# Optimization experiments

Measured on AMD Instinct MI355X. Metric: run time of the kernel, lower is better.

The kernel has to match this reference:

```python
import jax, jax.numpy as jnp
import numpy as np

NUM_TAGS = 48
B, S = 512, 2048


def setup_inputs() -> dict:
    key = jax.random.key(0)
    k1, k2, k3, k4, k5 = jax.random.split(key, 5)
    emissions = jax.random.normal(k1, (B, S, NUM_TAGS), dtype=jnp.float32)
    tags = jax.random.randint(k2, (B, S), 0, NUM_TAGS, dtype=jnp.int32)
    mask = jnp.ones((B, S), dtype=jnp.float32)
    transitions = jax.random.uniform(k3, (NUM_TAGS, NUM_TAGS), minval=-0.1, maxval=0.1, dtype=jnp.float32)
    start_transitions = jax.random.uniform(k4, (NUM_TAGS,), minval=-0.1, maxval=0.1, dtype=jnp.float32)
    end_transitions = jax.random.uniform(k5, (NUM_TAGS,), minval=-0.1, maxval=0.1, dtype=jnp.float32)
    return {"emissions": emissions, "transitions": transitions,
            "start_transitions": start_transitions, "end_transitions": end_transitions,
            "tags": tags, "mask": mask}


def reference(emissions, transitions, start_transitions, end_transitions, tags, mask):
    # emissions: [B,S,T], tags: [B,S] int, mask: [B,S] float (1 = valid)
    b, s, t = emissions.shape
    barange = jnp.arange(b)

    # ---- gold path score (fully vectorized over time) ----
    emit = jnp.take_along_axis(emissions, tags[:, :, None], axis=2)[..., 0]  # [B,S]
    score = start_transitions[tags[:, 0]] + emit[:, 0]
    trans = transitions[tags[:, :-1], tags[:, 1:]]                            # [B,S-1]
    score = score + jnp.sum((trans + emit[:, 1:]) * mask[:, 1:], axis=1)
    last_idx = mask.sum(axis=1).astype(jnp.int32) - 1
    last_tags = tags[barange, last_idx]
    score = score + end_transitions[last_tags]

    # ---- log-partition via forward algorithm (scan over time) ----
    alpha0 = start_transitions[None, :] + emissions[:, 0]                     # [B,T]

    def step(alpha, xs):
        emit_t, mask_t = xs                                                   # [B,T], [B]
        # scores[b,i,j] = alpha[b,i] + transitions[i,j] + emit_t[b,j]
        scores = alpha[:, :, None] + transitions[None, :, :] + emit_t[:, None, :]
        next_alpha = jax.nn.logsumexp(scores, axis=1)                         # [B,T]
        m = mask_t[:, None]
        alpha = next_alpha * m + alpha * (1.0 - m)
        return alpha, None

    xs = (jnp.swapaxes(emissions[:, 1:], 0, 1), jnp.swapaxes(mask[:, 1:], 0, 1))
    alpha, _ = jax.lax.scan(step, alpha0, xs)
    partition = jax.nn.logsumexp(alpha + end_transitions[None, :], axis=1)    # [B]

    return -jnp.mean(score - partition)
```

## Files before the change

### kernel.cpp

```cpp
#include <hip/hip_runtime.h>

#define NTAGS 48
#define NB    512
#define SLEN  2048

typedef float v2f __attribute__((ext_vector_type(2)));


__device__ __forceinline__ float rl_f(float v, int l) {
  return __builtin_bit_cast(float, __builtin_amdgcn_readlane(__builtin_bit_cast(int, v), l));
}

template <int CTRL, bool BC>
__device__ __forceinline__ float dpp_mv(float oldv, float v) {
  return __builtin_bit_cast(float, __builtin_amdgcn_update_dpp(
      __builtin_bit_cast(int, oldv), __builtin_bit_cast(int, v), CTRL, 0xF, 0xF, BC));
}

__device__ __forceinline__ float wred_max(float v) {
  v = fmaxf(v, dpp_mv<0x128, false>(v, v));
  v = fmaxf(v, dpp_mv<0x124, false>(v, v));
  v = fmaxf(v, dpp_mv<0x122, false>(v, v));
  v = fmaxf(v, dpp_mv<0x121, false>(v, v));
  v = fmaxf(v, dpp_mv<0x142, false>(v, v));
  v = fmaxf(v, dpp_mv<0x143, false>(v, v));
  return rl_f(v, 63);
}

__device__ __forceinline__ float wred_sum(float v) {
  v += dpp_mv<0x128, true>(0.0f, v);
  v += dpp_mv<0x124, true>(0.0f, v);
  v += dpp_mv<0x122, true>(0.0f, v);
  v += dpp_mv<0x121, true>(0.0f, v);
  v += dpp_mv<0x142, true>(0.0f, v);
  v += dpp_mv<0x143, true>(0.0f, v);
  return rl_f(v, 63);
}

__device__ __forceinline__ v2f fma2(v2f a, v2f b, v2f c) {
  return __builtin_elementwise_fma(a, b, c);
}

__device__ __forceinline__ float dot48(const float4* pv, const v2f* E2) {
  v2f a0 = {0.f, 0.f}, a1 = {0.f, 0.f}, a2 = {0.f, 0.f};
  v2f a3 = {0.f, 0.f}, a4 = {0.f, 0.f}, a5 = {0.f, 0.f};
#pragma unroll
  for (int k = 0; k < 4; ++k) {
    float4 x = pv[3 * k + 0];
    float4 y = pv[3 * k + 1];
    float4 z = pv[3 * k + 2];
    v2f xl = {x.x, x.y}, xh = {x.z, x.w};
    v2f yl = {y.x, y.y}, yh = {y.z, y.w};
    v2f zl = {z.x, z.y}, zh = {z.z, z.w};
    a0 = fma2(xl, E2[6 * k + 0], a0);
    a1 = fma2(xh, E2[6 * k + 1], a1);
    a2 = fma2(yl, E2[6 * k + 2], a2);
    a3 = fma2(yh, E2[6 * k + 3], a3);
    a4 = fma2(zl, E2[6 * k + 4], a4);
    a5 = fma2(zh, E2[6 * k + 5], a5);
  }
  v2f s = ((a0 + a1) + (a2 + a3)) + (a4 + a5);
  return s.x + s.y;
}

__device__ __forceinline__ void renorm(float& p, float& cl) {
  float mx = wred_max(p);
  int e = ((__builtin_bit_cast(int, mx) >> 23) & 255) - 127;
  float r = __builtin_bit_cast(float, (127 - e) << 23);
  p *= r;
  cl += (float)e * 0.6931471805599453f;
}


extern "C" __global__ __launch_bounds__(64, 1)
void crf_scan(const float* __restrict__ emis,
              const float* __restrict__ trans,
              const float* __restrict__ startt,
              const float* __restrict__ endt,
              const float* __restrict__ mask,
              float* __restrict__ wa, float* __restrict__ wb) {
  __shared__ __align__(16) float s_p[64];
  const int  lane = threadIdx.x;
  const int  bid  = blockIdx.x;
  const int  b    = bid >> 1;
  const bool fwd  = (bid & 1) == 0;
  const int  jc   = lane < NTAGS ? lane : (NTAGS - 1);

  const float* eb = emis + (size_t)b * SLEN * NTAGS;
  const float* mb = mask + (size_t)b * SLEN;

  v2f E2[24];
  if (fwd) {
#pragma unroll
    for (int i = 0; i < 24; ++i) {
      v2f e;
      e.x = __expf(trans[(2 * i + 0) * NTAGS + jc]);
      e.y = __expf(trans[(2 * i + 1) * NTAGS + jc]);
      E2[i] = e;
    }
  } else {
#pragma unroll
    for (int i = 0; i < 24; ++i) {
      v2f e;
      e.x = __expf(trans[jc * NTAGS + 2 * i + 0]);
      e.y = __expf(trans[jc * NTAGS + 2 * i + 1]);
      E2[i] = e;
    }
  }

  const float4* pv = (const float4*)s_p;
  float ebuf[8];
  float p, cl, een;

  if (fwd) {
    float a0 = startt[jc] + eb[jc];
    if (lane >= NTAGS) a0 = -1e30f;
    float m0 = wred_max(a0);
    p  = __expf(a0 - m0);
    cl = m0;
    s_p[lane] = p;
#pragma unroll
    for (int k = 1; k <= 8; ++k) ebuf[k & 7] = eb[(size_t)k * NTAGS + jc];
    een = __expf(ebuf[1]);

    for (int g = 0; g < 128; ++g) {
#pragma unroll
      for (int u = 0; u < 8; ++u) {
        const int t = 1 + 8 * g + u;
        float ee = een;
        een = __expf(ebuf[(t + 1) & 7]);
        float acc = dot48(pv, E2);
        float mv  = mb[t];
        float pn  = acc * ee;
        p = (mv != 0.0f) ? pn : p;
        ebuf[t & 7] = eb[(size_t)(t + 8) * NTAGS + jc];
        if (u == 7) renorm(p, cl);
        s_p[lane] = p;
      }
    }
    if (lane < NTAGS) wa[b * NTAGS + lane] = __logf(p) + cl;
  } else {
    float b0 = endt[jc];
    if (lane >= NTAGS) b0 = -1e30f;
    float m0 = wred_max(b0);
    p  = __expf(b0 - m0);
    cl = m0;
#pragma unroll
    for (int k = 0; k < 8; ++k) ebuf[(2047 - k) & 7] = eb[(size_t)(2047 - k) * NTAGS + jc];
    s_p[lane] = p * __expf(ebuf[7]);
    een = __expf(ebuf[6]);

#pragma unroll
    for (int pt = 0; pt < 7; ++pt) {
      const int t = 2047 - pt;
      float ee = een;
      een = __expf(ebuf[(t + 6) & 7]);
      float acc = dot48(pv, E2);
      float mv  = mb[t];
      p = (mv != 0.0f) ? acc : p;
      ebuf[t & 7] = eb[(size_t)(t - 8) * NTAGS + jc];
      if (pt == 6) renorm(p, cl);
      s_p[lane] = p * ee;
    }
    for (int g = 0; g < 127; ++g) {
#pragma unroll
      for (int u = 0; u < 8; ++u) {
        const int t = 2040 - 8 * g - u;
        float ee = een;
        een = __expf(ebuf[(t + 6) & 7]);
        float acc = dot48(pv, E2);
        float mv  = mb[t];
        p = (mv != 0.0f) ? acc : p;
        ebuf[t & 7] = eb[(size_t)(t - 8) * NTAGS + jc];
        if (u == 7) renorm(p, cl);
        s_p[lane] = p * ee;
      }
    }
    if (lane < NTAGS) wb[b * NTAGS + lane] = __logf(p) + cl;
  }
}


extern "C" __global__ __launch_bounds__(256)
void crf_score(const float* __restrict__ emis,
               const float* __restrict__ trans,
               const float* __restrict__ startt,
               const int*   __restrict__ tags,
               const float* __restrict__ mask,
               float* __restrict__ wsc, int* __restrict__ wcnt) {
  __shared__ float st[NTAGS * NTAGS];
  __shared__ float rs[4], rc[4];
  const int b   = blockIdx.x >> 3;
  const int seg = blockIdx.x & 7;
  const int tid = threadIdx.x;
  for (int k = tid; k < NTAGS * NTAGS; k += 256) st[k] = trans[k];
  __syncthreads();

  const int t = seg * 256 + tid;
  const int* tb = tags + (size_t)b * SLEN;
  float mv  = mask[(size_t)b * SLEN + t];
  int   cur = tb[t];
  float s, c = (mv != 0.0f) ? 1.0f : 0.0f;
  if (t == 0) {
    s = startt[cur] + emis[(size_t)b * SLEN * NTAGS + cur];
  } else {
    int prev = tb[t - 1];
    float ev = emis[((size_t)b * SLEN + t) * NTAGS + cur];
    s = (mv != 0.0f) ? (st[prev * NTAGS + cur] + ev) : 0.0f;
  }
  float ws_ = wred_sum(s);
  float wc_ = wred_sum(c);
  const int wid = tid >> 6;
  if ((tid & 63) == 0) { rs[wid] = ws_; rc[wid] = wc_; }
  __syncthreads();
  if (tid == 0) {
    wsc[blockIdx.x]  = rs[0] + rs[1] + rs[2] + rs[3];
    wcnt[blockIdx.x] = (int)(rc[0] + rc[1] + rc[2] + rc[3] + 0.5f);
  }
}


extern "C" __global__ __launch_bounds__(64)
void crf_combine(const float* __restrict__ wa, const float* __restrict__ wb,
                 const float* __restrict__ wsc, const int* __restrict__ wcnt,
                 const int* __restrict__ tags, const float* __restrict__ endt,
                 float* __restrict__ out) {
  const int b    = blockIdx.x;
  const int lane = threadIdx.x;
  float v = -1e30f;
  if (lane < NTAGS) v = wa[b * NTAGS + lane] + wb[b * NTAGS + lane];
  float m = wred_max(v);
  float s = wred_sum(__expf(v - m));
  float part = m + __logf(s);
  float sc = (lane < 8) ? wsc[b * 8 + lane] : 0.0f;
  float cf = (lane < 8) ? (float)wcnt[b * 8 + lane] : 0.0f;
  sc = wred_sum(sc);
  cf = wred_sum(cf);
  int last = (int)(cf + 0.5f) - 1;
  float score = sc + endt[tags[(size_t)b * SLEN + last]];
  if (lane == 0) atomicAdd(out, (part - score) * (1.0f / (float)NB));
}


extern "C" void kernel_launch(void* const* d_in, const int* in_sizes, int n_in,
                              void* d_out, int out_size, void* d_ws, size_t ws_size,
                              hipStream_t stream) {
  const float* emis  = (const float*)d_in[0];
  const float* trans = (const float*)d_in[1];
  const float* stt   = (const float*)d_in[2];
  const float* ent   = (const float*)d_in[3];
  const int*   tags  = (const int*)d_in[4];
  const float* mask  = (const float*)d_in[5];

  float* wa   = (float*)d_ws;
  float* wb   = wa + NB * NTAGS;
  float* wsc  = wb + NB * NTAGS;
  int*   wcnt = (int*)(wsc + NB * 8);

  hipMemsetAsync(d_out, 0, sizeof(float), stream);
  crf_scan<<<2 * NB, 64, 0, stream>>>(emis, trans, stt, ent, mask, wa, wb);
  crf_score<<<NB * 8, 256, 0, stream>>>(emis, trans, stt, tags, mask, wsc, wcnt);
  crf_combine<<<NB, 64, 0, stream>>>(wa, wb, wsc, wcnt, tags, ent, (float*)d_out);
}
```

Before: 481.5 us.

## Broadcast alpha via readlane instead of LDS and fuse gold-score kernel into scan

The forward/backward recurrence no longer writes alpha to shared memory and reads it back as float4. Each step instead broadcasts the 48 lane values with readlane into scalar operands and runs scalar FMAs against per-lane exp(transitions). This removes the LDS round trip and its wait on the serial critical path, but replaces packed v2f FMAs with 48 scalar FMAs plus readlanes per step. The gold-path score kernel is also merged into the same launch as extra 64-thread blocks, one per batch row looping over the sequence, which drops one kernel launch.

```diff
diff --git a/kernel.cpp b/kernel.cpp
--- a/kernel.cpp
+++ b/kernel.cpp
@@ -3,8 +3,6 @@
 #define NTAGS 48
 #define NB    512
 #define SLEN  2048
-
-typedef float v2f __attribute__((ext_vector_type(2)));
 
 
 __device__ __forceinline__ float rl_f(float v, int l) {
@@ -37,30 +35,16 @@
   return rl_f(v, 63);
 }
 
-__device__ __forceinline__ v2f fma2(v2f a, v2f b, v2f c) {
-  return __builtin_elementwise_fma(a, b, c);
-}
-
-__device__ __forceinline__ float dot48(const float4* pv, const v2f* E2) {
-  v2f a0 = {0.f, 0.f}, a1 = {0.f, 0.f}, a2 = {0.f, 0.f};
-  v2f a3 = {0.f, 0.f}, a4 = {0.f, 0.f}, a5 = {0.f, 0.f};
-#pragma unroll
-  for (int k = 0; k < 4; ++k) {
-    float4 x = pv[3 * k + 0];
-    float4 y = pv[3 * k + 1];
-    float4 z = pv[3 * k + 2];
-    v2f xl = {x.x, x.y}, xh = {x.z, x.w};
-    v2f yl = {y.x, y.y}, yh = {y.z, y.w};
-    v2f zl = {z.x, z.y}, zh = {z.z, z.w};
-    a0 = fma2(xl, E2[6 * k + 0], a0);
-    a1 = fma2(xh, E2[6 * k + 1], a1);
-    a2 = fma2(yl, E2[6 * k + 2], a2);
-    a3 = fma2(yh, E2[6 * k + 3], a3);
-    a4 = fma2(zl, E2[6 * k + 4], a4);
-    a5 = fma2(zh, E2[6 * k + 5], a5);
-  }
-  v2f s = ((a0 + a1) + (a2 + a3)) + (a4 + a5);
-  return s.x + s.y;
+__device__ __forceinline__ float rdot48(float v, const float* Ev) {
+  float a0 = 0.f, a1 = 0.f, a2 = 0.f, a3 = 0.f;
+#pragma unroll
+  for (int i = 0; i < NTAGS; i += 4) {
+    a0 = fmaf(rl_f(v, i + 0), Ev[i + 0], a0);
+    a1 = fmaf(rl_f(v, i + 1), Ev[i + 1], a1);
+    a2 = fmaf(rl_f(v, i + 2), Ev[i + 2], a2);
+    a3 = fmaf(rl_f(v, i + 3), Ev[i + 3], a3);
+  }
+  return (a0 + a1) + (a2 + a3);
 }
 
 __device__ __forceinline__ void renorm(float& p, float& cl) {
@@ -73,42 +57,61 @@
 
 
 extern "C" __global__ __launch_bounds__(64, 1)
-void crf_scan(const float* __restrict__ emis,
+void crf_main(const float* __restrict__ emis,
               const float* __restrict__ trans,
               const float* __restrict__ startt,
               const float* __restrict__ endt,
+              const int*   __restrict__ tags,
               const float* __restrict__ mask,
-              float* __restrict__ wa, float* __restrict__ wb) {
-  __shared__ __align__(16) float s_p[64];
-  const int  lane = threadIdx.x;
-  const int  bid  = blockIdx.x;
-  const int  b    = bid >> 1;
-  const bool fwd  = (bid & 1) == 0;
-  const int  jc   = lane < NTAGS ? lane : (NTAGS - 1);
+              float* __restrict__ wa, float* __restrict__ wb,
+              float* __restrict__ wsc, int* __restrict__ wcnt) {
+  __shared__ float st[NTAGS * NTAGS];
+  const int lane = threadIdx.x;
+  const int bid  = blockIdx.x;
+
+  if (bid >= 2 * NB) {
+    const int b = bid - 2 * NB;
+    for (int k = lane; k < NTAGS * NTAGS; k += 64) st[k] = trans[k];
+    __syncthreads();
+    const int* tb = tags + (size_t)b * SLEN;
+    float ssum = 0.0f, csum = 0.0f;
+    for (int it = 0; it < SLEN / 64; ++it) {
+      const int t   = it * 64 + lane;
+      int   cur = tb[t];
+      float mv  = mask[(size_t)b * SLEN + t];
+      float ev  = emis[((size_t)b * SLEN + t) * NTAGS + cur];
+      float s;
+      if (t == 0) {
+        s = startt[cur] + ev;
+      } else {
+        int prev = tb[t - 1];
+        s = (mv != 0.0f) ? (st[prev * NTAGS + cur] + ev) : 0.0f;
+      }
+      ssum += s;
+      csum += (mv != 0.0f) ? 1.0f : 0.0f;
+    }
+    ssum = wred_sum(ssum);
+    csum = wred_sum(csum);
+    if (lane == 0) { wsc[b] = ssum; wcnt[b] = (int)(csum + 0.5f); }
+    return;
+  }
+
+  const int  b   = bid >> 1;
+  const bool fwd = (bid & 1) == 0;
+  const int  jc  = lane < NTAGS ? lane : (NTAGS - 1);
 
   const float* eb = emis + (size_t)b * SLEN * NTAGS;
   const float* mb = mask + (size_t)b * SLEN;
 
-  v2f E2[24];
+  float Ev[NTAGS];
   if (fwd) {
 #pragma unroll
-    for (int i = 0; i < 24; ++i) {
-      v2f e;
-      e.x = __expf(trans[(2 * i + 0) * NTAGS + jc]);
-      e.y = __expf(trans[(2 * i + 1) * NTAGS + jc]);
-      E2[i] = e;
-    }
+    for (int i = 0; i < NTAGS; ++i) Ev[i] = __expf(trans[i * NTAGS + jc]);
   } else {
 #pragma unroll
-    for (int i = 0; i < 24; ++i) {
-      v2f e;
-      e.x = __expf(trans[jc * NTAGS + 2 * i + 0]);
-      e.y = __expf(trans[jc * NTAGS + 2 * i + 1]);
-      E2[i] = e;
-    }
-  }
-
-  const float4* pv = (const float4*)s_p;
+    for (int j = 0; j < NTAGS; ++j) Ev[j] = __expf(trans[jc * NTAGS + j]);
+  }
+
   float ebuf[8];
   float p, cl, een;
 
@@ -118,7 +121,6 @@
     float m0 = wred_max(a0);
     p  = __expf(a0 - m0);
     cl = m0;
-    s_p[lane] = p;
 #pragma unroll
     for (int k = 1; k <= 8; ++k) ebuf[k & 7] = eb[(size_t)k * NTAGS + jc];
     een = __expf(ebuf[1]);
@@ -129,13 +131,12 @@
         const int t = 1 + 8 * g + u;
         float ee = een;
         een = __expf(ebuf[(t + 1) & 7]);
-        float acc = dot48(pv, E2);
+        float acc = rdot48(p, Ev);
         float mv  = mb[t];
         float pn  = acc * ee;
         p = (mv != 0.0f) ? pn : p;
         ebuf[t & 7] = eb[(size_t)(t + 8) * NTAGS + jc];
         if (u == 7) renorm(p, cl);
-        s_p[lane] = p;
       }
     }
     if (lane < NTAGS) wa[b * NTAGS + lane] = __logf(p) + cl;
@@ -147,7 +148,7 @@
     cl = m0;
 #pragma unroll
     for (int k = 0; k < 8; ++k) ebuf[(2047 - k) & 7] = eb[(size_t)(2047 - k) * NTAGS + jc];
-    s_p[lane] = p * __expf(ebuf[7]);
+    float q = p * __expf(ebuf[7]);
     een = __expf(ebuf[6]);
 
 #pragma unroll
@@ -155,12 +156,12 @@
       const int t = 2047 - pt;
       float ee = een;
       een = __expf(ebuf[(t + 6) & 7]);
-      float acc = dot48(pv, E2);
+      float acc = rdot48(q, Ev);
       float mv  = mb[t];
       p = (mv != 0.0f) ? acc : p;
       ebuf[t & 7] = eb[(size_t)(t - 8) * NTAGS + jc];
       if (pt == 6) renorm(p, cl);
-      s_p[lane] = p * ee;
+      q = p * ee;
     }
     for (int g = 0; g < 127; ++g) {
 #pragma unroll
@@ -168,54 +169,15 @@
         const int t = 2040 - 8 * g - u;
         float ee = een;
         een = __expf(ebuf[(t + 6) & 7]);
-        float acc = dot48(pv, E2);
+        float acc = rdot48(q, Ev);
         float mv  = mb[t];
         p = (mv != 0.0f) ? acc : p;
         ebuf[t & 7] = eb[(size_t)(t - 8) * NTAGS + jc];
         if (u == 7) renorm(p, cl);
-        s_p[lane] = p * ee;
+        q = p * ee;
       }
     }
     if (lane < NTAGS) wb[b * NTAGS + lane] = __logf(p) + cl;
-  }
-}
-
-
-extern "C" __global__ __launch_bounds__(256)
-void crf_score(const float* __restrict__ emis,
-               const float* __restrict__ trans,
-               const float* __restrict__ startt,
-               const int*   __restrict__ tags,
-               const float* __restrict__ mask,
-               float* __restrict__ wsc, int* __restrict__ wcnt) {
-  __shared__ float st[NTAGS * NTAGS];
-  __shared__ float rs[4], rc[4];
-  const int b   = blockIdx.x >> 3;
-  const int seg = blockIdx.x & 7;
-  const int tid = threadIdx.x;
-  for (int k = tid; k < NTAGS * NTAGS; k += 256) st[k] = trans[k];
-  __syncthreads();
-
-  const int t = seg * 256 + tid;
-  const int* tb = tags + (size_t)b * SLEN;
-  float mv  = mask[(size_t)b * SLEN + t];
-  int   cur = tb[t];
-  float s, c = (mv != 0.0f) ? 1.0f : 0.0f;
-  if (t == 0) {
-    s = startt[cur] + emis[(size_t)b * SLEN * NTAGS + cur];
-  } else {
-    int prev = tb[t - 1];
-    float ev = emis[((size_t)b * SLEN + t) * NTAGS + cur];
-    s = (mv != 0.0f) ? (st[prev * NTAGS + cur] + ev) : 0.0f;
-  }
-  float ws_ = wred_sum(s);
-  float wc_ = wred_sum(c);
-  const int wid = tid >> 6;
-  if ((tid & 63) == 0) { rs[wid] = ws_; rc[wid] = wc_; }
-  __syncthreads();
-  if (tid == 0) {
-    wsc[blockIdx.x]  = rs[0] + rs[1] + rs[2] + rs[3];
-    wcnt[blockIdx.x] = (int)(rc[0] + rc[1] + rc[2] + rc[3] + 0.5f);
   }
 }
 
@@ -232,12 +194,8 @@
   float m = wred_max(v);
   float s = wred_sum(__expf(v - m));
   float part = m + __logf(s);
-  float sc = (lane < 8) ? wsc[b * 8 + lane] : 0.0f;
-  float cf = (lane < 8) ? (float)wcnt[b * 8 + lane] : 0.0f;
-  sc = wred_sum(sc);
-  cf = wred_sum(cf);
-  int last = (int)(cf + 0.5f) - 1;
-  float score = sc + endt[tags[(size_t)b * SLEN + last]];
+  int   last = wcnt[b] - 1;
+  float score = wsc[b] + endt[tags[(size_t)b * SLEN + last]];
   if (lane == 0) atomicAdd(out, (part - score) * (1.0f / (float)NB));
 }
 
@@ -255,10 +213,10 @@
   float* wa   = (float*)d_ws;
   float* wb   = wa + NB * NTAGS;
   float* wsc  = wb + NB * NTAGS;
-  int*   wcnt = (int*)(wsc + NB * 8);
+  int*   wcnt = (int*)(wsc + NB);
 
   hipMemsetAsync(d_out, 0, sizeof(float), stream);
-  crf_scan<<<2 * NB, 64, 0, stream>>>(emis, trans, stt, ent, mask, wa, wb);
-  crf_score<<<NB * 8, 256, 0, stream>>>(emis, trans, stt, tags, mask, wsc, wcnt);
+  crf_main<<<2 * NB + NB, 64, 0, stream>>>(emis, trans, stt, ent, tags, mask,
+                                           wa, wb, wsc, wcnt);
   crf_combine<<<NB, 64, 0, stream>>>(wa, wb, wsc, wcnt, tags, ent, (float*)d_out);
 }
```

Result: faster. 425.4 us (-11.7%).
